# Kernel optimization log

Hardware: AMD Instinct MI355X
Metric: run time of the kernel (lower is better)

## Reference

```python
import jax, jax.numpy as jnp
import numpy as np

NEG_SLOPE = 0.2


def gat_conv(x, src, dst, W, a_src, a_dst, b, heads, ch, n_nodes):
    # x: [N, F_in] -> h: [N, H, C]
    h = (x @ W).reshape(n_nodes, heads, ch)
    alpha_src = (h * a_src).sum(-1)  # [N, H]
    alpha_dst = (h * a_dst).sum(-1)  # [N, H]
    e = jax.nn.leaky_relu(alpha_src[src] + alpha_dst[dst], NEG_SLOPE)  # [E, H]
    # segment softmax over destination neighborhoods (every node has a self-loop)
    m = jax.ops.segment_max(e, dst, num_segments=n_nodes)
    e = jnp.exp(e - m[dst])
    s = jax.ops.segment_sum(e, dst, num_segments=n_nodes)
    alpha = e / s[dst]  # [E, H]
    out = jax.ops.segment_sum(h[src] * alpha[:, :, None], dst, num_segments=n_nodes)
    return out.reshape(n_nodes, heads * ch) + b


def setup_inputs() -> dict:
    key = jax.random.key(0)
    ks = jax.random.split(key, 12)
    N, E = 50000, 800000
    F_in, HID, H, OUT = 128, 64, 2, 64
    x = jax.random.normal(ks[0], (N, F_in), dtype=jnp.float32)
    edge_index = jax.random.randint(ks[1], (2, E), 0, N, dtype=jnp.int64)
    s1 = 1.0 / np.sqrt(F_in)
    s2 = 1.0 / np.sqrt(H * HID)
    return {
        "x": x,
        "edge_index": edge_index,
        "W1": jax.random.normal(ks[2], (F_in, H * HID), dtype=jnp.float32) * s1,
        "att_src1": jax.random.normal(ks[3], (H, HID), dtype=jnp.float32) * s1,
        "att_dst1": jax.random.normal(ks[4], (H, HID), dtype=jnp.float32) * s1,
        "b1": jnp.zeros((H * HID,), dtype=jnp.float32),
        "W2": jax.random.normal(ks[5], (H * HID, OUT), dtype=jnp.float32) * s2,
        "att_src2": jax.random.normal(ks[6], (1, OUT), dtype=jnp.float32) * s2,
        "att_dst2": jax.random.normal(ks[7], (1, OUT), dtype=jnp.float32) * s2,
        "b2": jnp.zeros((OUT,), dtype=jnp.float32),
    }


def reference(x, edge_index, W1, att_src1, att_dst1, b1, W2, att_src2, att_dst2, b2):
    N = x.shape[0]
    # PyG GATConv adds self-loops by default
    loops = jnp.arange(N, dtype=edge_index.dtype)
    src = jnp.concatenate([edge_index[0], loops])
    dst = jnp.concatenate([edge_index[1], loops])
    h = gat_conv(x, src, dst, W1, att_src1, att_dst1, b1, 2, 64, N)
    h = jax.nn.relu(h)
    out = gat_conv(h, src, dst, W2, att_src2, att_dst2, b2, 1, 64, N)
    return jax.nn.sigmoid(out)
```

## Files before the change

kernel.cpp:

```cpp
#include <hip/hip_runtime.h>
#include <math.h>

#define N_NODES 50000
#define N_EDGES 800000
#define E_TOT   (N_EDGES + N_NODES)
#define NEG_SLOPE 0.2f
#define NB_BKT  ((N_NODES + 127) / 128)
#define BKT_CAP 3200
#define P1_CHUNK 4096
#define NB_P1   ((E_TOT + P1_CHUNK - 1) / P1_CHUNK)
#define NB_G1   ((N_NODES + 127) / 128)

typedef short bf16x8 __attribute__((ext_vector_type(8)));
typedef float f32x4 __attribute__((ext_vector_type(4)));

static __device__ __forceinline__ float lrelu(float v) {
    return v > 0.0f ? v : NEG_SLOPE * v;
}

static __device__ __forceinline__ unsigned short f2bf(float f) {
    unsigned b = __float_as_uint(f);
    return (unsigned short)((b + 0x7fffu + ((b >> 16) & 1u)) >> 16);
}

static __device__ __forceinline__ float bflo(unsigned u) { return __uint_as_float(u << 16); }
static __device__ __forceinline__ float bfhi(unsigned u) { return __uint_as_float(u & 0xffff0000u); }

static __device__ __forceinline__ int swz(int row, int k) {
    return row * 128 + ((((k >> 3) ^ (row & 15)) << 3) | (k & 7));
}
static __device__ __forceinline__ int swz64(int row, int c) {
    return row * 64 + ((((c >> 3) ^ (row & 7)) << 3) | (c & 7));
}

__global__ __launch_bounds__(256, 2) void fusedA_kernel(const float* __restrict__ x,
                                                        const float* __restrict__ W,
                                                        const float* __restrict__ a_src,
                                                        const float* __restrict__ a_dst,
                                                        unsigned short* __restrict__ h1b,
                                                        float* __restrict__ as_out,
                                                        float* __restrict__ ad_out,
                                                        const int* __restrict__ ei,
                                                        int* __restrict__ bktcnt,
                                                        uint2* __restrict__ pairs) {
    __shared__ __align__(16) unsigned char smem[65536];
    int tid = threadIdx.x;

    if (blockIdx.x >= NB_G1) {
        int* cnt  = (int*)smem;
        int* base = (int*)(smem + 2048);
        for (int i = tid; i < NB_BKT; i += 256) cnt[i] = 0;
        __syncthreads();
        int cbase = (blockIdx.x - NB_G1) * P1_CHUNK;
        for (int i = tid; i < P1_CHUNK; i += 256) {
            int e = cbase + i;
            if (e >= E_TOT) break;
            int d = (e < N_EDGES) ? ei[N_EDGES + e] : (e - N_EDGES);
            atomicAdd(&cnt[d >> 7], 1);
        }
        __syncthreads();
        for (int i = tid; i < NB_BKT; i += 256) {
            int c = cnt[i];
            base[i] = c ? (BKT_CAP * i + atomicAdd(&bktcnt[i], c)) : 0;
            cnt[i] = 0;
        }
        __syncthreads();
        for (int i = tid; i < P1_CHUNK; i += 256) {
            int e = cbase + i;
            if (e >= E_TOT) break;
            int s, d;
            if (e < N_EDGES) { s = ei[e]; d = ei[N_EDGES + e]; }
            else { s = d = e - N_EDGES; }
            int bk = d >> 7;
            int p = base[bk] + atomicAdd(&cnt[bk], 1);
            pairs[p] = make_uint2((unsigned)s, (unsigned)d);
        }
        return;
    }

    unsigned short* xs = (unsigned short*)smem;
    unsigned short* wt = (unsigned short*)(smem + 32768);
    int r0 = blockIdx.x * 128;

    {
        int n = tid & 127;
        int c0 = (tid >> 7) * 8;
        for (int c = c0; c < c0 + 8; ++c) {
            int kb = c * 8;
            ushort4 lo, hi;
            lo.x = f2bf(W[(kb + 0) * 128 + n]);
            lo.y = f2bf(W[(kb + 1) * 128 + n]);
            lo.z = f2bf(W[(kb + 2) * 128 + n]);
            lo.w = f2bf(W[(kb + 3) * 128 + n]);
            hi.x = f2bf(W[(kb + 4) * 128 + n]);
            hi.y = f2bf(W[(kb + 5) * 128 + n]);
            hi.z = f2bf(W[(kb + 6) * 128 + n]);
            hi.w = f2bf(W[(kb + 7) * 128 + n]);
            int a = swz(n, kb);
            *(ushort4*)&wt[a] = lo;
            *(ushort4*)&wt[a + 4] = hi;
        }
    }
    {
        const int maxe = N_NODES * 128 - 4;
#pragma unroll
        for (int i = 0; i < 16384; i += 1024) {
            int e = i + tid * 4;
            int ge = r0 * 128 + e;
            if (ge > maxe) ge = maxe;
            float4 v = *(const float4*)&x[ge];
            ushort4 p;
            p.x = f2bf(v.x); p.y = f2bf(v.y); p.z = f2bf(v.z); p.w = f2bf(v.w);
            *(ushort4*)&xs[swz(e >> 7, e & 127)] = p;
        }
    }
    __syncthreads();

    int wv = tid >> 6, lane = tid & 63, lm = lane & 15, quad = lane >> 4;
    f32x4 acc[2][8];
#pragma unroll
    for (int m = 0; m < 2; ++m)
#pragma unroll
        for (int n = 0; n < 8; ++n) acc[m][n] = (f32x4){0.f, 0.f, 0.f, 0.f};

#pragma unroll
    for (int kc = 0; kc < 4; ++kc) {
        int kb = kc * 32 + quad * 8;
        bf16x8 a0 = *(bf16x8*)&xs[swz(wv * 32 + lm, kb)];
        bf16x8 a1 = *(bf16x8*)&xs[swz(wv * 32 + 16 + lm, kb)];
#pragma unroll
        for (int nt = 0; nt < 8; ++nt) {
            bf16x8 b = *(bf16x8*)&wt[swz(nt * 16 + lm, kb)];
            acc[0][nt] = __builtin_amdgcn_mfma_f32_16x16x32_bf16(a0, b, acc[0][nt], 0, 0, 0);
            acc[1][nt] = __builtin_amdgcn_mfma_f32_16x16x32_bf16(a1, b, acc[1][nt], 0, 0, 0);
        }
    }

    float asv[8], adv[8];
#pragma unroll
    for (int nt = 0; nt < 8; ++nt) {
        asv[nt] = a_src[nt * 16 + lm];
        adv[nt] = a_dst[nt * 16 + lm];
    }
#pragma unroll
    for (int mt = 0; mt < 2; ++mt) {
#pragma unroll
        for (int r = 0; r < 4; ++r) {
            float s0 = 0.f, s1 = 0.f, d0 = 0.f, d1 = 0.f;
#pragma unroll
            for (int nt = 0; nt < 4; ++nt) {
                s0 += acc[mt][nt][r] * asv[nt];
                d0 += acc[mt][nt][r] * adv[nt];
            }
#pragma unroll
            for (int nt = 4; nt < 8; ++nt) {
                s1 += acc[mt][nt][r] * asv[nt];
                d1 += acc[mt][nt][r] * adv[nt];
            }
#pragma unroll
            for (int m = 1; m < 16; m <<= 1) {
                s0 += __shfl_xor(s0, m, 64);
                s1 += __shfl_xor(s1, m, 64);
                d0 += __shfl_xor(d0, m, 64);
                d1 += __shfl_xor(d1, m, 64);
            }
            if (lm == 0) {
                int gr = r0 + wv * 32 + mt * 16 + quad * 4 + r;
                if (gr < N_NODES) {
                    as_out[gr * 2 + 0] = s0;
                    as_out[gr * 2 + 1] = s1;
                    ad_out[gr * 2 + 0] = d0;
                    ad_out[gr * 2 + 1] = d1;
                }
            }
        }
    }

    __syncthreads();
#pragma unroll
    for (int mt = 0; mt < 2; ++mt) {
#pragma unroll
        for (int nt = 0; nt < 8; ++nt) {
#pragma unroll
            for (int r = 0; r < 4; ++r) {
                int lrow = wv * 32 + mt * 16 + quad * 4 + r;
                xs[swz(lrow, nt * 16 + lm)] = f2bf(acc[mt][nt][r]);
            }
        }
    }
    __syncthreads();
    {
        int lrow = tid >> 1;
        int cb = (tid & 1) * 64;
        int gr = r0 + lrow;
        if (gr < N_NODES) {
            unsigned short* dst = h1b + (size_t)gr * 128 + cb;
#pragma unroll
            for (int c = 0; c < 8; ++c)
                *(uint4*)(dst + c * 8) = *(uint4*)&xs[swz(lrow, cb + c * 8)];
        }
    }
}

__global__ __launch_bounds__(256) void scatterP2_kernel(const uint2* __restrict__ pairs,
                                 const int* __restrict__ bktcnt,
                                 int* __restrict__ offsets, int* __restrict__ deg,
                                 int* __restrict__ csr_src) {
    __shared__ int cnt[256];
    __shared__ int scn[256];
    __shared__ int sst[256];
    __shared__ int lsrc[BKT_CAP];
    int t = threadIdx.x;
    int b = blockIdx.x;
    int node0 = b << 7;
    int pbase = b * BKT_CAP;
    int cntE = bktcnt[b];
    cnt[t] = 0;
    __syncthreads();
    for (int j = t; j < cntE; j += 256)
        atomicAdd(&cnt[pairs[pbase + j].y - node0], 1);
    __syncthreads();
    int v = cnt[t];
    scn[t] = v;
    __syncthreads();
#pragma unroll
    for (int off = 1; off < 256; off <<= 1) {
        int u = (t >= off) ? scn[t - off] : 0;
        __syncthreads();
        scn[t] += u;
        __syncthreads();
    }
    int lstart = scn[t] - v;
    sst[t] = lstart;
    cnt[t] = lstart;
    if (t < 128 && node0 + t < N_NODES) {
        offsets[node0 + t] = pbase + lstart;
        deg[node0 + t] = v;
    }
    __syncthreads();
    for (int j = t; j < cntE; j += 256) {
        uint2 pr = pairs[pbase + j];
        int dl = (int)pr.y - node0;
        int p = atomicAdd(&cnt[dl], 1);
        lsrc[p] = ((int)pr.x << 8) | dl;
    }
    __syncthreads();
    for (int j = t; j < cntE; j += 256) {
        int w = lsrc[j];
        int dl = w & 255;
        int st = sst[dl];
        int en = scn[dl];
        int r = 0;
        for (int k = st; k < en; ++k) {
            int wk = lsrc[k];
            r += (wk < w) ? 1 : ((wk == w && k < j) ? 1 : 0);
        }
        csr_src[pbase + st + r] = ((unsigned)w) >> 8;
    }
}

__global__ __launch_bounds__(256, 2) void gemm2_kernel(const unsigned short* __restrict__ xb,
                                                       const float* __restrict__ W,
                                                       const float* __restrict__ a_src,
                                                       const float* __restrict__ a_dst,
                                                       unsigned short* __restrict__ h2b,
                                                       float* __restrict__ as_out,
                                                       float* __restrict__ ad_out) {
    __shared__ unsigned short xs[128 * 128];
    __shared__ unsigned short wt[64 * 128];
    int tid = threadIdx.x;
    int r0 = blockIdx.x * 128;

    {
        int n = tid & 63;
        int c0 = (tid >> 6) * 4;
        for (int c = c0; c < c0 + 4; ++c) {
            int kb = c * 8;
            ushort4 lo, hi;
            lo.x = f2bf(W[(kb + 0) * 64 + n]);
            lo.y = f2bf(W[(kb + 1) * 64 + n]);
            lo.z = f2bf(W[(kb + 2) * 64 + n]);
            lo.w = f2bf(W[(kb + 3) * 64 + n]);
            hi.x = f2bf(W[(kb + 4) * 64 + n]);
            hi.y = f2bf(W[(kb + 5) * 64 + n]);
            hi.z = f2bf(W[(kb + 6) * 64 + n]);
            hi.w = f2bf(W[(kb + 7) * 64 + n]);
            int a = swz(n, kb);
            *(ushort4*)&wt[a] = lo;
            *(ushort4*)&wt[a + 4] = hi;
        }
    }
    {
        const int maxe = N_NODES * 128 - 8;
#pragma unroll
        for (int i = 0; i < 16384; i += 2048) {
            int e = i + tid * 8;
            int ge = r0 * 128 + e;
            if (ge > maxe) ge = maxe;
            uint4 v = *(const uint4*)&xb[ge];
            *(uint4*)&xs[swz(e >> 7, e & 127)] = v;
        }
    }
    __syncthreads();

    int wv = tid >> 6, lane = tid & 63, lm = lane & 15, quad = lane >> 4;
    f32x4 acc[2][4];
#pragma unroll
    for (int m = 0; m < 2; ++m)
#pragma unroll
        for (int n = 0; n < 4; ++n) acc[m][n] = (f32x4){0.f, 0.f, 0.f, 0.f};

#pragma unroll
    for (int kc = 0; kc < 4; ++kc) {
        int kb = kc * 32 + quad * 8;
        bf16x8 a0 = *(bf16x8*)&xs[swz(wv * 32 + lm, kb)];
        bf16x8 a1 = *(bf16x8*)&xs[swz(wv * 32 + 16 + lm, kb)];
#pragma unroll
        for (int nt = 0; nt < 4; ++nt) {
            bf16x8 b = *(bf16x8*)&wt[swz(nt * 16 + lm, kb)];
            acc[0][nt] = __builtin_amdgcn_mfma_f32_16x16x32_bf16(a0, b, acc[0][nt], 0, 0, 0);
            acc[1][nt] = __builtin_amdgcn_mfma_f32_16x16x32_bf16(a1, b, acc[1][nt], 0, 0, 0);
        }
    }

    float asv[4], adv[4];
#pragma unroll
    for (int nt = 0; nt < 4; ++nt) {
        asv[nt] = a_src[nt * 16 + lm];
        adv[nt] = a_dst[nt * 16 + lm];
    }
#pragma unroll
    for (int mt = 0; mt < 2; ++mt) {
#pragma unroll
        for (int r = 0; r < 4; ++r) {
            float s0 = 0.f, d0 = 0.f;
#pragma unroll
            for (int nt = 0; nt < 4; ++nt) {
                s0 += acc[mt][nt][r] * asv[nt];
                d0 += acc[mt][nt][r] * adv[nt];
            }
#pragma unroll
            for (int m = 1; m < 16; m <<= 1) {
                s0 += __shfl_xor(s0, m, 64);
                d0 += __shfl_xor(d0, m, 64);
            }
            if (lm == 0) {
                int gr = r0 + wv * 32 + mt * 16 + quad * 4 + r;
                if (gr < N_NODES) {
                    as_out[gr] = s0;
                    ad_out[gr] = d0;
                }
            }
        }
    }

    __syncthreads();
#pragma unroll
    for (int mt = 0; mt < 2; ++mt) {
#pragma unroll
        for (int nt = 0; nt < 4; ++nt) {
#pragma unroll
            for (int r = 0; r < 4; ++r) {
                int lrow = wv * 32 + mt * 16 + quad * 4 + r;
                wt[swz64(lrow, nt * 16 + lm)] = f2bf(acc[mt][nt][r]);
            }
        }
    }
    __syncthreads();
    {
        int lrow = tid >> 1;
        int cb = (tid & 1) * 32;
        int gr = r0 + lrow;
        if (gr < N_NODES) {
            unsigned short* dst = h2b + (size_t)gr * 64 + cb;
#pragma unroll
            for (int c = 0; c < 4; ++c)
                *(uint4*)(dst + c * 8) = *(uint4*)&wt[swz64(lrow, cb + c * 8)];
        }
    }
}

__global__ void agg1_kernel(const unsigned short* __restrict__ h1b,
                            const float* __restrict__ as1,
                            const float* __restrict__ ad1, const float* __restrict__ b1,
                            const int* __restrict__ offsets, const int* __restrict__ deg,
                            const int* __restrict__ csr_src,
                            unsigned short* __restrict__ out1b) {
    int wid = (blockIdx.x * blockDim.x + threadIdx.x) >> 6;
    if (wid >= N_NODES) return;
    int lane = threadIdx.x & 63;
    int cl = lane & 31;
    int half = lane >> 5;
    bool head1 = (cl >= 16);
    float da0 = ad1[wid * 2 + 0], da1 = ad1[wid * 2 + 1];
    int jb = offsets[wid], je = jb + deg[wid];
    float a0 = 0.f, a1 = 0.f, a2 = 0.f, a3 = 0.f;
    float psum0 = 0.f, psum1 = 0.f;

    for (int chunk = jb; chunk < je; chunk += 64) {
        int j = chunk + lane;
        int s = 0; float w0 = 0.f, w1 = 0.f;
        if (j < je) {
            s = csr_src[j];
            float2 av = *(const float2*)&as1[s * 2];
            w0 = __expf(lrelu(av.x + da0));
            w1 = __expf(lrelu(av.y + da1));
        }
        psum0 += w0; psum1 += w1;
        int cnt = je - chunk; if (cnt > 64) cnt = 64;
        for (int k = 0; k < cnt; k += 8) {
            int k0 = k + half, k1 = k + 2 + half, k2 = k + 4 + half, k3 = k + 6 + half;
            int ss0 = __shfl(s, k0, 64);
            int ss1 = __shfl(s, k1, 64);
            int ss2 = __shfl(s, k2, 64);
            int ss3 = __shfl(s, k3, 64);
            uint2 u0 = ((const uint2*)(h1b + (size_t)ss0 * 128))[cl];
            uint2 u1 = ((const uint2*)(h1b + (size_t)ss1 * 128))[cl];
            uint2 u2 = ((const uint2*)(h1b + (size_t)ss2 * 128))[cl];
            uint2 u3 = ((const uint2*)(h1b + (size_t)ss3 * 128))[cl];
            float p0 = __shfl(w0, k0, 64), q0 = __shfl(w1, k0, 64);
            float p1 = __shfl(w0, k1, 64), q1 = __shfl(w1, k1, 64);
            float p2 = __shfl(w0, k2, 64), q2 = __shfl(w1, k2, 64);
            float p3 = __shfl(w0, k3, 64), q3 = __shfl(w1, k3, 64);
            float bw0 = head1 ? q0 : p0;
            float bw1 = head1 ? q1 : p1;
            float bw2 = head1 ? q2 : p2;
            float bw3 = head1 ? q3 : p3;
            a0 += bw0 * bflo(u0.x); a1 += bw0 * bfhi(u0.x); a2 += bw0 * bflo(u0.y); a3 += bw0 * bfhi(u0.y);
            a0 += bw1 * bflo(u1.x); a1 += bw1 * bfhi(u1.x); a2 += bw1 * bflo(u1.y); a3 += bw1 * bfhi(u1.y);
            a0 += bw2 * bflo(u2.x); a1 += bw2 * bfhi(u2.x); a2 += bw2 * bflo(u2.y); a3 += bw2 * bfhi(u2.y);
            a0 += bw3 * bflo(u3.x); a1 += bw3 * bfhi(u3.x); a2 += bw3 * bflo(u3.y); a3 += bw3 * bfhi(u3.y);
        }
    }
#pragma unroll
    for (int m = 1; m < 64; m <<= 1) {
        psum0 += __shfl_xor(psum0, m, 64);
        psum1 += __shfl_xor(psum1, m, 64);
    }
    float o0 = __shfl(a0, cl + 32, 64);
    float o1 = __shfl(a1, cl + 32, 64);
    float o2 = __shfl(a2, cl + 32, 64);
    float o3 = __shfl(a3, cl + 32, 64);
    if (lane < 32) {
        float inv = 1.f / (head1 ? psum1 : psum0);
        float4 bv = *(const float4*)&b1[cl * 4];
        float v0 = (a0 + o0) * inv + bv.x;
        float v1 = (a1 + o1) * inv + bv.y;
        float v2 = (a2 + o2) * inv + bv.z;
        float v3 = (a3 + o3) * inv + bv.w;
        v0 = v0 > 0.f ? v0 : 0.f;
        v1 = v1 > 0.f ? v1 : 0.f;
        v2 = v2 > 0.f ? v2 : 0.f;
        v3 = v3 > 0.f ? v3 : 0.f;
        ushort4 p;
        p.x = f2bf(v0); p.y = f2bf(v1); p.z = f2bf(v2); p.w = f2bf(v3);
        *(ushort4*)&out1b[(size_t)wid * 128 + cl * 4] = p;
    }
}

__global__ void agg2_kernel(const unsigned short* __restrict__ h2b,
                            const float* __restrict__ as2,
                            const float* __restrict__ ad2, const float* __restrict__ b2,
                            const int* __restrict__ offsets, const int* __restrict__ deg,
                            const int* __restrict__ csr_src,
                            float* __restrict__ out) {
    int wid = (blockIdx.x * blockDim.x + threadIdx.x) >> 6;
    if (wid >= N_NODES) return;
    int lane = threadIdx.x & 63;
    int cl = lane & 31;
    int half = lane >> 5;
    float da = ad2[wid];
    int jb = offsets[wid], je = jb + deg[wid];
    float acc0 = 0.f, acc1 = 0.f, psum = 0.f;

    for (int chunk = jb; chunk < je; chunk += 64) {
        int j = chunk + lane;
        int s = 0; float w = 0.f;
        if (j < je) {
            s = csr_src[j];
            w = __expf(lrelu(as2[s] + da));
        }
        psum += w;
        int cnt = je - chunk; if (cnt > 64) cnt = 64;
        for (int k = 0; k < cnt; k += 8) {
            int k0 = k + half, k1 = k + 2 + half, k2 = k + 4 + half, k3 = k + 6 + half;
            int ss0 = __shfl(s, k0, 64);
            int ss1 = __shfl(s, k1, 64);
            int ss2 = __shfl(s, k2, 64);
            int ss3 = __shfl(s, k3, 64);
            unsigned u0 = ((const unsigned*)(h2b + (size_t)ss0 * 64))[cl];
            unsigned u1 = ((const unsigned*)(h2b + (size_t)ss1 * 64))[cl];
            unsigned u2 = ((const unsigned*)(h2b + (size_t)ss2 * 64))[cl];
            unsigned u3 = ((const unsigned*)(h2b + (size_t)ss3 * 64))[cl];
            float bw0 = __shfl(w, k0, 64);
            float bw1 = __shfl(w, k1, 64);
            float bw2 = __shfl(w, k2, 64);
            float bw3 = __shfl(w, k3, 64);
            acc0 += bw0 * bflo(u0); acc1 += bw0 * bfhi(u0);
            acc0 += bw1 * bflo(u1); acc1 += bw1 * bfhi(u1);
            acc0 += bw2 * bflo(u2); acc1 += bw2 * bfhi(u2);
            acc0 += bw3 * bflo(u3); acc1 += bw3 * bfhi(u3);
        }
    }
#pragma unroll
    for (int m = 1; m < 64; m <<= 1) psum += __shfl_xor(psum, m, 64);
    float o0 = __shfl(acc0, cl + 32, 64);
    float o1 = __shfl(acc1, cl + 32, 64);
    if (lane < 32) {
        float inv = 1.f / psum;
        float2 bv = *(const float2*)&b2[cl * 2];
        float v0 = (acc0 + o0) * inv + bv.x;
        float v1 = (acc1 + o1) * inv + bv.y;
        v0 = 1.f / (1.f + __expf(-v0));
        v1 = 1.f / (1.f + __expf(-v1));
        *(float2*)&out[(size_t)wid * 64 + cl * 2] = make_float2(v0, v1);
    }
}

extern "C" void kernel_launch(void* const* d_in, const int* in_sizes, int n_in,
                              void* d_out, int out_size, void* d_ws, size_t ws_size,
                              hipStream_t stream) {
    const float* x     = (const float*)d_in[0];
    const int*   ei    = (const int*)d_in[1];
    const float* W1    = (const float*)d_in[2];
    const float* asrc1 = (const float*)d_in[3];
    const float* adst1 = (const float*)d_in[4];
    const float* b1    = (const float*)d_in[5];
    const float* W2    = (const float*)d_in[6];
    const float* asrc2 = (const float*)d_in[7];
    const float* adst2 = (const float*)d_in[8];
    const float* b2    = (const float*)d_in[9];
    float* out = (float*)d_out;

    float* ws = (float*)d_ws;
    size_t off = 0;
    float* as1  = ws + off; off += (size_t)N_NODES * 2;
    float* ad1  = ws + off; off += (size_t)N_NODES * 2;
    float* as2  = ws + off; off += (size_t)N_NODES;
    float* ad2  = ws + off; off += (size_t)N_NODES;
    unsigned short* h1b   = (unsigned short*)(ws + off); off += (size_t)N_NODES * 64;
    unsigned short* out1b = (unsigned short*)(ws + off); off += (size_t)N_NODES * 64;
    unsigned short* h2b   = (unsigned short*)(ws + off); off += (size_t)N_NODES * 32;
    int* offsets = (int*)(ws + off);
    int* deg     = offsets + N_NODES;
    int* csr_src = deg + N_NODES;
    int* bktcnt  = csr_src + NB_BKT * BKT_CAP;
    uint2* pairs = (uint2*)((((size_t)(bktcnt + NB_BKT)) + 7) & ~(size_t)7);

    hipMemsetAsync(bktcnt, 0, NB_BKT * sizeof(int), stream);

    fusedA_kernel<<<NB_G1 + NB_P1, 256, 0, stream>>>(x, W1, asrc1, adst1, h1b, as1, ad1,
                                                     ei, bktcnt, pairs);
    scatterP2_kernel<<<NB_BKT, 256, 0, stream>>>(pairs, bktcnt, offsets, deg, csr_src);
    agg1_kernel<<<(N_NODES * 64 + 255) / 256, 256, 0, stream>>>(h1b, as1, ad1, b1, offsets, deg, csr_src, out1b);
    gemm2_kernel<<<NB_G1, 256, 0, stream>>>(out1b, W2, asrc2, adst2, h2b, as2, ad2);
    agg2_kernel<<<(N_NODES * 64 + 255) / 256, 256, 0, stream>>>(h2b, as2, ad2, b2, offsets, deg, csr_src, out);
}
```

Before: 201.8 us.

## Pretranspose weights in prep kernel, pack edge pairs, split agg1 across two waves

Adds a small prep kernel that zeroes bucket counters and pre-converts W1/W2 to transposed bf16, so the GEMM blocks load weights with vector copies instead of strided scalar converts. The separate memset launch goes away. Edge pairs are packed into one 32-bit word (src<<7 | local dst), halving pair traffic. agg1 now uses two waves per node, each taking alternate 8-edge groups, with the partial sums combined through shared memory and a block barrier. The cost is one extra launch and a syncthreads in agg1.

Result: slower. 220.1 us (+9.1%).

```diff
diff --git a/kernel.cpp b/kernel.cpp
--- a/kernel.cpp
+++ b/kernel.cpp
@@ -33,8 +33,33 @@
     return row * 64 + ((((c >> 3) ^ (row & 7)) << 3) | (c & 7));
 }
 
+__global__ __launch_bounds__(256) void prep_kernel(const float* __restrict__ W1,
+                                                   const float* __restrict__ W2,
+                                                   unsigned short* __restrict__ w1t,
+                                                   unsigned short* __restrict__ w2t,
+                                                   int* __restrict__ bktcnt) {
+    int tid = threadIdx.x;
+    int b = blockIdx.x;
+    if (b == 0) {
+        for (int i = tid; i < NB_BKT; i += 256) bktcnt[i] = 0;
+    } else if (b <= 2) {
+        int k0 = (b - 1) * 64;
+        for (int idx = tid; idx < 64 * 128; idx += 256) {
+            int k = k0 + (idx >> 7);
+            int n = idx & 127;
+            w1t[n * 128 + k] = f2bf(W1[k * 128 + n]);
+        }
+    } else {
+        for (int idx = tid; idx < 128 * 64; idx += 256) {
+            int k = idx >> 6;
+            int n = idx & 63;
+            w2t[n * 128 + k] = f2bf(W2[k * 64 + n]);
+        }
+    }
+}
+
 __global__ __launch_bounds__(256, 2) void fusedA_kernel(const float* __restrict__ x,
-                                                        const float* __restrict__ W,
+                                                        const unsigned short* __restrict__ w1t,
                                                         const float* __restrict__ a_src,
                                                         const float* __restrict__ a_dst,
                                                         unsigned short* __restrict__ h1b,
@@ -42,7 +67,7 @@
                                                         float* __restrict__ ad_out,
                                                         const int* __restrict__ ei,
                                                         int* __restrict__ bktcnt,
-                                                        uint2* __restrict__ pairs) {
+                                                        unsigned* __restrict__ pairs) {
     __shared__ __align__(16) unsigned char smem[65536];
     int tid = threadIdx.x;
 
@@ -73,7 +98,7 @@
             else { s = d = e - N_EDGES; }
             int bk = d >> 7;
             int p = base[bk] + atomicAdd(&cnt[bk], 1);
-            pairs[p] = make_uint2((unsigned)s, (unsigned)d);
+            pairs[p] = ((unsigned)s << 7) | (unsigned)(d & 127);
         }
         return;
     }
@@ -87,18 +112,8 @@
         int c0 = (tid >> 7) * 8;
         for (int c = c0; c < c0 + 8; ++c) {
             int kb = c * 8;
-            ushort4 lo, hi;
-            lo.x = f2bf(W[(kb + 0) * 128 + n]);
-            lo.y = f2bf(W[(kb + 1) * 128 + n]);
-            lo.z = f2bf(W[(kb + 2) * 128 + n]);
-            lo.w = f2bf(W[(kb + 3) * 128 + n]);
-            hi.x = f2bf(W[(kb + 4) * 128 + n]);
-            hi.y = f2bf(W[(kb + 5) * 128 + n]);
-            hi.z = f2bf(W[(kb + 6) * 128 + n]);
-            hi.w = f2bf(W[(kb + 7) * 128 + n]);
-            int a = swz(n, kb);
-            *(ushort4*)&wt[a] = lo;
-            *(ushort4*)&wt[a + 4] = hi;
+            uint4 v = *(const uint4*)&w1t[n * 128 + kb];
+            *(uint4*)&wt[swz(n, kb)] = v;
         }
     }
     {
@@ -202,7 +217,7 @@
     }
 }
 
-__global__ __launch_bounds__(256) void scatterP2_kernel(const uint2* __restrict__ pairs,
+__global__ __launch_bounds__(256) void scatterP2_kernel(const unsigned* __restrict__ pairs,
                                  const int* __restrict__ bktcnt,
                                  int* __restrict__ offsets, int* __restrict__ deg,
                                  int* __restrict__ csr_src) {
@@ -218,7 +233,7 @@
     cnt[t] = 0;
     __syncthreads();
     for (int j = t; j < cntE; j += 256)
-        atomicAdd(&cnt[pairs[pbase + j].y - node0], 1);
+        atomicAdd(&cnt[pairs[pbase + j] & 127u], 1);
     __syncthreads();
     int v = cnt[t];
     scn[t] = v;
@@ -239,15 +254,15 @@
     }
     __syncthreads();
     for (int j = t; j < cntE; j += 256) {
-        uint2 pr = pairs[pbase + j];
-        int dl = (int)pr.y - node0;
+        unsigned w = pairs[pbase + j];
+        int dl = (int)(w & 127u);
         int p = atomicAdd(&cnt[dl], 1);
-        lsrc[p] = ((int)pr.x << 8) | dl;
+        lsrc[p] = (int)w;
     }
     __syncthreads();
     for (int j = t; j < cntE; j += 256) {
         int w = lsrc[j];
-        int dl = w & 255;
+        int dl = w & 127;
         int st = sst[dl];
         int en = scn[dl];
         int r = 0;
@@ -255,12 +270,12 @@
             int wk = lsrc[k];
             r += (wk < w) ? 1 : ((wk == w && k < j) ? 1 : 0);
         }
-        csr_src[pbase + st + r] = ((unsigned)w) >> 8;
+        csr_src[pbase + st + r] = (int)(((unsigned)w) >> 7);
     }
 }
 
 __global__ __launch_bounds__(256, 2) void gemm2_kernel(const unsigned short* __restrict__ xb,
-                                                       const float* __restrict__ W,
+                                                       const unsigned short* __restrict__ w2t,
                                                        const float* __restrict__ a_src,
                                                        const float* __restrict__ a_dst,
                                                        unsigned short* __restrict__ h2b,
@@ -276,18 +291,8 @@
         int c0 = (tid >> 6) * 4;
         for (int c = c0; c < c0 + 4; ++c) {
             int kb = c * 8;
-            ushort4 lo, hi;
-            lo.x = f2bf(W[(kb + 0) * 64 + n]);
-            lo.y = f2bf(W[(kb + 1) * 64 + n]);
-            lo.z = f2bf(W[(kb + 2) * 64 + n]);
-            lo.w = f2bf(W[(kb + 3) * 64 + n]);
-            hi.x = f2bf(W[(kb + 4) * 64 + n]);
-            hi.y = f2bf(W[(kb + 5) * 64 + n]);
-            hi.z = f2bf(W[(kb + 6) * 64 + n]);
-            hi.w = f2bf(W[(kb + 7) * 64 + n]);
-            int a = swz(n, kb);
-            *(ushort4*)&wt[a] = lo;
-            *(ushort4*)&wt[a + 4] = hi;
+            uint4 v = *(const uint4*)&w2t[n * 128 + kb];
+            *(uint4*)&wt[swz(n, kb)] = v;
         }
     }
     {
@@ -386,9 +391,12 @@
                             const int* __restrict__ offsets, const int* __restrict__ deg,
                             const int* __restrict__ csr_src,
                             unsigned short* __restrict__ out1b) {
-    int wid = (blockIdx.x * blockDim.x + threadIdx.x) >> 6;
-    if (wid >= N_NODES) return;
-    int lane = threadIdx.x & 63;
+    __shared__ float xacc[2][32][4];
+    int tid = threadIdx.x;
+    int nib = tid >> 7;
+    int wid = blockIdx.x * 2 + nib;
+    int sub = (tid >> 6) & 1;
+    int lane = tid & 63;
     int cl = lane & 31;
     int half = lane >> 5;
     bool head1 = (cl >= 16);
@@ -408,7 +416,7 @@
         }
         psum0 += w0; psum1 += w1;
         int cnt = je - chunk; if (cnt > 64) cnt = 64;
-        for (int k = 0; k < cnt; k += 8) {
+        for (int k = 8 * sub; k < cnt; k += 16) {
             int k0 = k + half, k1 = k + 2 + half, k2 = k + 4 + half, k3 = k + 6 + half;
             int ss0 = __shfl(s, k0, 64);
             int ss1 = __shfl(s, k1, 64);
@@ -441,13 +449,20 @@
     float o1 = __shfl(a1, cl + 32, 64);
     float o2 = __shfl(a2, cl + 32, 64);
     float o3 = __shfl(a3, cl + 32, 64);
-    if (lane < 32) {
+    float t0 = 0.f, t1 = 0.f, t2 = 0.f, t3 = 0.f;
+    if (lane < 32) { t0 = a0 + o0; t1 = a1 + o1; t2 = a2 + o2; t3 = a3 + o3; }
+    if (sub == 1 && lane < 32) {
+        xacc[nib][cl][0] = t0; xacc[nib][cl][1] = t1;
+        xacc[nib][cl][2] = t2; xacc[nib][cl][3] = t3;
+    }
+    __syncthreads();
+    if (sub == 0 && lane < 32) {
         float inv = 1.f / (head1 ? psum1 : psum0);
         float4 bv = *(const float4*)&b1[cl * 4];
-        float v0 = (a0 + o0) * inv + bv.x;
-        float v1 = (a1 + o1) * inv + bv.y;
-        float v2 = (a2 + o2) * inv + bv.z;
-        float v3 = (a3 + o3) * inv + bv.w;
+        float v0 = (t0 + xacc[nib][cl][0]) * inv + bv.x;
+        float v1 = (t1 + xacc[nib][cl][1]) * inv + bv.y;
+        float v2 = (t2 + xacc[nib][cl][2]) * inv + bv.z;
+        float v3 = (t3 + xacc[nib][cl][3]) * inv + bv.w;
         v0 = v0 > 0.f ? v0 : 0.f;
         v1 = v1 > 0.f ? v1 : 0.f;
         v2 = v2 > 0.f ? v2 : 0.f;
@@ -541,18 +556,19 @@
     unsigned short* h1b   = (unsigned short*)(ws + off); off += (size_t)N_NODES * 64;
     unsigned short* out1b = (unsigned short*)(ws + off); off += (size_t)N_NODES * 64;
     unsigned short* h2b   = (unsigned short*)(ws + off); off += (size_t)N_NODES * 32;
+    unsigned short* w1t   = (unsigned short*)(ws + off); off += 8192;
+    unsigned short* w2t   = (unsigned short*)(ws + off); off += 4096;
     int* offsets = (int*)(ws + off);
     int* deg     = offsets + N_NODES;
     int* csr_src = deg + N_NODES;
     int* bktcnt  = csr_src + NB_BKT * BKT_CAP;
-    uint2* pairs = (uint2*)((((size_t)(bktcnt + NB_BKT)) + 7) & ~(size_t)7);
-
-    hipMemsetAsync(bktcnt, 0, NB_BKT * sizeof(int), stream);
-
-    fusedA_kernel<<<NB_G1 + NB_P1, 256, 0, stream>>>(x, W1, asrc1, adst1, h1b, as1, ad1,
+    unsigned* pairs = (unsigned*)(bktcnt + NB_BKT);
+
+    prep_kernel<<<4, 256, 0, stream>>>(W1, W2, w1t, w2t, bktcnt);
+    fusedA_kernel<<<NB_G1 + NB_P1, 256, 0, stream>>>(x, w1t, asrc1, adst1, h1b, as1, ad1,
                                                      ei, bktcnt, pairs);
     scatterP2_kernel<<<NB_BKT, 256, 0, stream>>>(pairs, bktcnt, offsets, deg, csr_src);
-    agg1_kernel<<<(N_NODES * 64 + 255) / 256, 256, 0, stream>>>(h1b, as1, ad1, b1, offsets, deg, csr_src, out1b);
-    gemm2_kernel<<<NB_G1, 256, 0, stream>>>(out1b, W2, asrc2, adst2, h2b, as2, ad2);
+    agg1_kernel<<<N_NODES / 2, 256, 0, stream>>>(h1b, as1, ad1, b1, offsets, deg, csr_src, out1b);
+    gemm2_kernel<<<NB_G1, 256, 0, stream>>>(out1b, w2t, asrc2, adst2, h2b, as2, ad2);
     agg2_kernel<<<(N_NODES * 64 + 255) / 256, 256, 0, stream>>>(h2b, as2, ad2, b2, offsets, deg, csr_src, out);
 }
```
